# Optimization experiments

Measured on AMD Instinct MI355X. Metric: run time of the kernel, lower is better.

The kernel has to match this reference:

```python
import jax, jax.numpy as jnp
import numpy as np

D = 64          # d_model
H = 128         # ffn_hidden_dim
N = 10000       # nodes
E = 50000       # edges
NEG_SLOPE = 0.01  # LeakyReLU default


def setup_inputs() -> dict:
    key = jax.random.key(0)
    ks = jax.random.split(key, 10)
    x = jax.random.normal(ks[0], (N, D), dtype=jnp.float32)
    edge_index = jax.random.randint(ks[1], (2, E), 0, N)
    edge_attr = jax.random.normal(ks[2], (E, D), dtype=jnp.float32)
    # MapE2NxN params (stored as [in, out] so forward is x @ W + b)
    w1 = jax.random.normal(ks[3], (D, H), dtype=jnp.float32) / np.sqrt(D)
    b1 = jnp.zeros((H,), dtype=jnp.float32)
    w2 = jax.random.normal(ks[4], (H, D * D), dtype=jnp.float32) / np.sqrt(H)
    b2 = jnp.zeros((D * D,), dtype=jnp.float32)
    # NNConv root weight + bias
    root = jax.random.normal(ks[5], (D, D), dtype=jnp.float32) / np.sqrt(D)
    bias = jnp.zeros((D,), dtype=jnp.float32)
    # LayerNorm affine params
    gamma = jnp.ones((D,), dtype=jnp.float32)
    beta = jnp.zeros((D,), dtype=jnp.float32)
    return {"x": x, "edge_attr": edge_attr, "gamma": gamma, "beta": beta,
            "w1": w1, "b1": b1, "w2": w2, "b2": b2,
            "root": root, "bias": bias, "edge_index": edge_index}


def _layer_norm(h, gamma, beta, eps=1e-5):
    mu = jnp.mean(h, axis=-1, keepdims=True)
    var = jnp.var(h, axis=-1, keepdims=True)
    return (h - mu) * jax.lax.rsqrt(var + eps) * gamma + beta


def _leaky_relu(h):
    return jnp.where(h >= 0, h, NEG_SLOPE * h)


def reference(x, edge_attr, gamma, beta, w1, b1, w2, b2, root, bias, edge_index):
    src, dst = edge_index[0], edge_index[1]
    # DeepGCNLayer block='res+': pre-activation norm -> act -> (dropout p=0) -> conv -> residual
    h = _leaky_relu(_layer_norm(x, gamma, beta))
    # MapE2NxN on edge attributes -> per-edge [D, D] weight matrix
    we = _leaky_relu(edge_attr @ w1 + b1) @ w2 + b2   # [E, D*D]
    we = we.reshape(E, D, D)
    # per-edge matvec with source node features (PyG NNConv message)
    msg = jnp.einsum('ed,edf->ef', h[src], we)        # [E, D]
    # scatter-mean aggregate into destination nodes
    agg = jax.ops.segment_sum(msg, dst, num_segments=N)
    cnt = jax.ops.segment_sum(jnp.ones((E,), dtype=msg.dtype), dst, num_segments=N)
    agg = agg / jnp.maximum(cnt, 1.0)[:, None]
    # root transform + bias, then residual
    out = agg + h @ root + bias
    return x + out
```

## Files before the change

### kernel.cpp

```cpp
#include <hip/hip_runtime.h>

#define NS 10000
#define DD 64
#define HH 128
#define EE 50000
#define SLOPE 0.01f
#define BPAD 8448
#define NCH 33

typedef __attribute__((ext_vector_type(8))) short short8;
typedef __attribute__((ext_vector_type(4))) short bf4;
typedef __attribute__((ext_vector_type(4))) float f32x4;

static __device__ __forceinline__ unsigned short f2bf(float f) {
  unsigned int u = __float_as_uint(f);
  u += 0x7fff + ((u >> 16) & 1);
  return (unsigned short)(u >> 16);
}
static __device__ __forceinline__ float bf2f(unsigned short s) {
  return __uint_as_float((unsigned int)s << 16);
}
static __device__ __forceinline__ unsigned cvtpk(float lo, float hi) {
  unsigned r;
  asm("v_cvt_pk_bf16_f32 %0, %1, %2" : "=v"(r) : "v"(lo), "v"(hi));
  return r;
}

__device__ __forceinline__ float wave_sum64(float v) {
  #pragma unroll
  for (int m = 32; m >= 1; m >>= 1) v += __shfl_xor(v, m, 64);
  return v;
}

#define TBLK 128
#define PBLK 2500
#define UB 782
__global__ __launch_bounds__(256) void k_prep(const float* __restrict__ x,
    const float* __restrict__ gamma, const float* __restrict__ beta,
    float* __restrict__ h, unsigned short* __restrict__ hbf,
    const float* __restrict__ ea, const float* __restrict__ w2,
    unsigned short* __restrict__ w2e, const float* __restrict__ w1,
    const float* __restrict__ b1, unsigned short* __restrict__ ubf,
    const float* __restrict__ b2, const int* __restrict__ ei,
    int* __restrict__ cntdst) {
  __shared__ __align__(16) unsigned char smem[18432];
  int t = threadIdx.x;
  int bid = blockIdx.x;
  if (bid < TBLK) {
    float (*tile)[65] = (float(*)[65])smem;
    int k = bid;
    #pragma unroll
    for (int i = 0; i < 16; ++i) {
      int idx = t + i * 256;
      tile[idx >> 6][idx & 63] = w2[k * (DD * DD) + idx];
    }
    __syncthreads();
    #pragma unroll
    for (int it = 0; it < 2; ++it) {
      int slot = t + it * 256;
      int f = slot >> 3, l8 = slot & 7;
      short8 o;
      #pragma unroll
      for (int j = 0; j < 8; ++j) o[j] = f2bf(tile[l8 * 8 + j][f]);
      *(short8*)(w2e + (size_t)f * BPAD + k * DD + l8 * 8) = o;
    }
    return;
  }
  if (bid == TBLK) {
    #pragma unroll
    for (int i = 0; i < 16; ++i) {
      int idx = t + i * 256;
      int d = idx >> 6, f = idx & 63;
      w2e[(size_t)f * BPAD + 8192 + d] = f2bf(b2[idx]);
    }
    #pragma unroll
    for (int i = 0; i < 6; ++i) {
      int slot = t + i * 256;
      int f = slot / 24, z8 = slot % 24;
      short8 z = {};
      *(short8*)(w2e + (size_t)f * BPAD + 8256 + z8 * 8) = z;
    }
    return;
  }
  if (bid < TBLK + 1 + PBLK) {
    int pbid = bid - TBLK - 1;
    int gid = pbid * 256 + t;
    if (gid < EE) atomicAdd(&cntdst[ei[EE + gid]], 1);
    int wid = t >> 6;
    int lane = t & 63;
    int row = pbid * 4 + wid;
    if (row >= NS) return;
    float v = x[row * DD + lane];
    float s = wave_sum64(v);
    float s2 = wave_sum64(v * v);
    float mu = s * (1.0f / 64.0f);
    float var = s2 * (1.0f / 64.0f) - mu * mu;
    float r = rsqrtf(var + 1e-5f);
    float hn = (v - mu) * r * gamma[lane] + beta[lane];
    float hv = hn >= 0.f ? hn : SLOPE * hn;
    h[row * DD + lane] = hv;
    hbf[row * DD + lane] = f2bf(hv);
    return;
  }
  int ublk = bid - TBLK - 1 - PBLK;
  unsigned short (*W)[72] = (unsigned short(*)[72])smem;
  int w = t >> 6, lane = t & 63, lr = lane & 15, lg = lane >> 4;
  int r0 = ublk * 64 + w * 16;
  int ra = r0 + lr; if (ra >= EE) ra = EE - 1;
  const float* ep = ea + (size_t)ra * DD;
  float4 e0 = *(const float4*)(ep + lg * 8);
  float4 e1 = *(const float4*)(ep + lg * 8 + 4);
  float4 e2 = *(const float4*)(ep + 32 + lg * 8);
  float4 e3 = *(const float4*)(ep + 32 + lg * 8 + 4);
  #pragma unroll
  for (int i = 0; i < 32; ++i) {
    int idx = t + i * 256;
    int d = idx >> 7, hc = idx & 127;
    W[hc][d] = f2bf(w1[idx]);
  }
  __syncthreads();
  short8 a0, a1;
  a0[0] = f2bf(e0.x); a0[1] = f2bf(e0.y); a0[2] = f2bf(e0.z); a0[3] = f2bf(e0.w);
  a0[4] = f2bf(e1.x); a0[5] = f2bf(e1.y); a0[6] = f2bf(e1.z); a0[7] = f2bf(e1.w);
  a1[0] = f2bf(e2.x); a1[1] = f2bf(e2.y); a1[2] = f2bf(e2.z); a1[3] = f2bf(e2.w);
  a1[4] = f2bf(e3.x); a1[5] = f2bf(e3.y); a1[6] = f2bf(e3.z); a1[7] = f2bf(e3.w);
  short8 bb0[8], bb1[8];
  #pragma unroll
  for (int ni = 0; ni < 8; ++ni) {
    bb0[ni] = *(const short8*)(&W[ni * 16 + lr][lg * 8]);
    bb1[ni] = *(const short8*)(&W[ni * 16 + lr][32 + lg * 8]);
  }
  f32x4 acc[8] = {};
  #pragma unroll
  for (int ni = 0; ni < 8; ++ni) {
    acc[ni] = __builtin_amdgcn_mfma_f32_16x16x32_bf16(a0, bb0[ni], acc[ni], 0, 0, 0);
    acc[ni] = __builtin_amdgcn_mfma_f32_16x16x32_bf16(a1, bb1[ni], acc[ni], 0, 0, 0);
  }
  #pragma unroll
  for (int ni = 0; ni < 8; ++ni) {
    int col = ni * 16 + lr;
    float bb = b1[col];
    #pragma unroll
    for (int reg = 0; reg < 4; ++reg) {
      int gr = r0 + lg * 4 + reg;
      if (gr < EE) {
        float vv = acc[ni][reg] + bb;
        ubf[(size_t)gr * HH + col] = f2bf(vv >= 0.f ? vv : SLOPE * vv);
      }
    }
  }
}

__global__ __launch_bounds__(256) void k_msgd(
    const unsigned short* __restrict__ ubf, const float* __restrict__ hf,
    const unsigned short* __restrict__ w2e, const int* __restrict__ ei,
    float* __restrict__ agg) {
  __shared__ unsigned short Bs[64 * 256];
  int t = threadIdx.x;
  int w = t >> 6, lane = t & 63, lr = lane & 15, lg = lane >> 4;
  int cq = blockIdx.y;
  int nch = (cq == 3) ? 9 : 8;
  int ebase = (blockIdx.x * 4 + w) * 32;
  int e0 = ebase + lr, e1 = ebase + 16 + lr;
  int e0c = e0 < EE ? e0 : EE - 1;
  int e1c = e1 < EE ? e1 : EE - 1;
  int s0 = ei[e0c], s1 = ei[e1c];
  float h0[2][8], h1[2][8];
  #pragma unroll
  for (int par = 0; par < 2; ++par) {
    const float* p0 = hf + (size_t)s0 * DD + par * 32 + lg * 8;
    const float* p1 = hf + (size_t)s1 * DD + par * 32 + lg * 8;
    *(float4*)(&h0[par][0]) = *(const float4*)(p0);
    *(float4*)(&h0[par][4]) = *(const float4*)(p0 + 4);
    *(float4*)(&h1[par][0]) = *(const float4*)(p1);
    *(float4*)(&h1[par][4]) = *(const float4*)(p1 + 4);
  }
  const unsigned short* u0 = ubf + (size_t)e0c * HH;
  const unsigned short* u1 = ubf + (size_t)e1c * HH;
  int sf = (t >> 4);
  int so8 = (t & 15);
  short8 sreg[8];
  {
    int ch0 = cq * 8;
    #pragma unroll
    for (int i = 0; i < 8; ++i) {
      int f = sf + (i & 3) * 16;
      int o8 = so8 + (i >> 2) * 16;
      sreg[i] = *(const short8*)(w2e + (size_t)f * BPAD + ch0 * 256 + o8 * 8);
    }
  }
  f32x4 acc[2][4] = {};
  for (int ci = 0; ci < nch; ++ci) {
    int ch = (ci < 8) ? (cq * 8 + ci) : 32;
    __syncthreads();
    #pragma unroll
    for (int i = 0; i < 8; ++i) {
      int f = sf + (i & 3) * 16;
      int o8 = so8 + (i >> 2) * 16;
      *(short8*)(&Bs[f * 256 + (o8 ^ (f & 7)) * 8]) = sreg[i];
    }
    if (ci + 1 < nch) {
      int ch2 = (ci + 1 < 8) ? (cq * 8 + ci + 1) : 32;
      #pragma unroll
      for (int i = 0; i < 8; ++i) {
        int f = sf + (i & 3) * 16;
        int o8 = so8 + (i >> 2) * 16;
        sreg[i] = *(const short8*)(w2e + (size_t)f * BPAD + ch2 * 256 + o8 * 8);
      }
    }
    float uf0[4], uf1[4];
    if (ch < 32) {
      bf4 v0 = *(const bf4*)(u0 + ch * 4);
      bf4 v1 = *(const bf4*)(u1 + ch * 4);
      #pragma unroll
      for (int kk = 0; kk < 4; ++kk) {
        uf0[kk] = bf2f((unsigned short)v0[kk]);
        uf1[kk] = bf2f((unsigned short)v1[kk]);
      }
    } else {
      uf0[0] = 1.f; uf0[1] = 0.f; uf0[2] = 0.f; uf0[3] = 0.f;
      uf1[0] = 1.f; uf1[1] = 0.f; uf1[2] = 0.f; uf1[3] = 0.f;
    }
    __syncthreads();
    #pragma unroll
    for (int ks = 0; ks < 8; ++ks) {
      int par = ks & 1;
      float u0k = (ks >> 1) == 0 ? uf0[0] : (ks >> 1) == 1 ? uf0[1]
                 : (ks >> 1) == 2 ? uf0[2] : uf0[3];
      float u1k = (ks >> 1) == 0 ? uf1[0] : (ks >> 1) == 1 ? uf1[1]
                 : (ks >> 1) == 2 ? uf1[2] : uf1[3];
      union { unsigned u[4]; short8 s; } pk0, pk1;
      #pragma unroll
      for (int jj = 0; jj < 4; ++jj) {
        pk0.u[jj] = cvtpk(u0k * h0[par][jj * 2], u0k * h0[par][jj * 2 + 1]);
        pk1.u[jj] = cvtpk(u1k * h1[par][jj * 2], u1k * h1[par][jj * 2 + 1]);
      }
      int o8r = ks * 4 + lg;
      #pragma unroll
      for (int ft = 0; ft < 4; ++ft) {
        int f = ft * 16 + lr;
        short8 b = *(const short8*)(&Bs[f * 256 + (o8r ^ (f & 7)) * 8]);
        acc[0][ft] = __builtin_amdgcn_mfma_f32_16x16x32_bf16(pk0.s, b,
                                                             acc[0][ft], 0, 0, 0);
        acc[1][ft] = __builtin_amdgcn_mfma_f32_16x16x32_bf16(pk1.s, b,
                                                             acc[1][ft], 0, 0, 0);
      }
    }
  }
  #pragma unroll
  for (int m = 0; m < 2; ++m)
    #pragma unroll
    for (int reg = 0; reg < 4; ++reg) {
      int ee = ebase + m * 16 + lg * 4 + reg;
      if (ee < EE) {
        int dstn = ei[EE + ee];
        #pragma unroll
        for (int ft = 0; ft < 4; ++ft)
          atomicAdd(&agg[(size_t)dstn * DD + ft * 16 + lr],
                    m == 0 ? acc[0][ft][reg] : acc[1][ft][reg]);
      }
    }
}

__global__ __launch_bounds__(256) void k_final(const float* __restrict__ x,
    const float* __restrict__ h, const float* __restrict__ root,
    const float* __restrict__ bias, const float* __restrict__ agg,
    const int* __restrict__ cnt, float* __restrict__ out) {
  __shared__ float Bs[DD][DD + 1];
  __shared__ float As[32][DD];
  int t = threadIdx.x;
  #pragma unroll
  for (int i = 0; i < 16; ++i) {
    int idx = t + i * 256;
    Bs[idx >> 6][idx & 63] = root[idx];
  }
  int row0 = blockIdx.x * 32;
  #pragma unroll
  for (int i = 0; i < 8; ++i) {
    int idx = t + i * 256;
    int r = idx >> 6, d = idx & 63;
    int gr = row0 + r;
    As[r][d] = (gr < NS) ? h[gr * DD + d] : 0.f;
  }
  __syncthreads();
  int r = t >> 3;
  int c0 = (t & 7) * 8;
  int gr = row0 + r;
  if (gr >= NS) return;
  float acc[8] = {};
  for (int d = 0; d < DD; ++d) {
    float a = As[r][d];
    #pragma unroll
    for (int j = 0; j < 8; ++j) acc[j] += a * Bs[d][c0 + j];
  }
  float inv = 1.0f / fmaxf((float)cnt[gr], 1.0f);
  #pragma unroll
  for (int j = 0; j < 8; ++j) {
    size_t gi = (size_t)gr * DD + c0 + j;
    out[gi] = x[gi] + agg[gi] * inv + acc[j] + bias[c0 + j];
  }
}

extern "C" void kernel_launch(void* const* d_in, const int* in_sizes, int n_in,
                              void* d_out, int out_size, void* d_ws, size_t ws_size,
                              hipStream_t stream) {
  const float* x     = (const float*)d_in[0];
  const float* ea    = (const float*)d_in[1];
  const float* gamma = (const float*)d_in[2];
  const float* beta  = (const float*)d_in[3];
  const float* w1    = (const float*)d_in[4];
  const float* b1    = (const float*)d_in[5];
  const float* w2    = (const float*)d_in[6];
  const float* b2    = (const float*)d_in[7];
  const float* root  = (const float*)d_in[8];
  const float* bias  = (const float*)d_in[9];
  const int*   ei    = (const int*)d_in[10];
  float* out = (float*)d_out;

  char* p = (char*)d_ws;
  auto carve = [&](size_t bytes) {
    char* q = p;
    p += (bytes + 255) & ~(size_t)255;
    return q;
  };
  float* h            = (float*)carve(sizeof(float) * NS * DD);
  unsigned short* hbf = (unsigned short*)carve(sizeof(short) * NS * DD);
  unsigned short* w2e = (unsigned short*)carve(sizeof(short) * (size_t)DD * BPAD);
  unsigned short* ubf = (unsigned short*)carve(sizeof(short) * (size_t)EE * HH);
  char* z0 = p;
  float* agg          = (float*)carve(sizeof(float) * NS * DD);
  int* cntdst         = (int*)carve(sizeof(int) * NS);
  size_t zlen = (size_t)(p - z0);

  (void)hipMemsetAsync(z0, 0, zlen, stream);
  k_prep<<<dim3(TBLK + 1 + PBLK + UB), dim3(256), 0, stream>>>(
      x, gamma, beta, h, hbf, ea, w2, w2e, w1, b1, ubf, b2, ei, cntdst);
  k_msgd<<<dim3((EE + 127) / 128, 4), dim3(256), 0, stream>>>(
      ubf, h, w2e, ei, agg);
  k_final<<<dim3((NS + 31) / 32), dim3(256), 0, stream>>>(x, h, root, bias, agg,
                                                          cntdst, out);
}
```

Measured before the change: 122.3 us.

## Switch message kernel to fp16 packed products and split chunks across eight groups

Intermediates (h, u, expanded w2) are now stored as fp16 instead of bf16/fp32. The per-edge A operand is built with packed fp16 multiplies instead of fp32 multiplies plus bf16 conversion, and the MFMA becomes the f16 variant. The k_msgd grid doubles along y (8 chunk groups of 4 instead of 4 of 8), and the u values are preloaded up front, to raise parallelism and cut per-iteration conversion work. The cost is fewer MFMA chunks per block, more atomic adds into agg, and fp16 range and precision risk on u*h products.

```diff
diff --git a/kernel.cpp b/kernel.cpp
--- a/kernel.cpp
+++ b/kernel.cpp
@@ -6,10 +6,9 @@
 #define EE 50000
 #define SLOPE 0.01f
 #define BPAD 8448
-#define NCH 33
 
 typedef __attribute__((ext_vector_type(8))) short short8;
-typedef __attribute__((ext_vector_type(4))) short bf4;
+typedef __attribute__((ext_vector_type(8))) _Float16 half8;
 typedef __attribute__((ext_vector_type(4))) float f32x4;
 
 static __device__ __forceinline__ unsigned short f2bf(float f) {
@@ -17,13 +16,20 @@
   u += 0x7fff + ((u >> 16) & 1);
   return (unsigned short)(u >> 16);
 }
-static __device__ __forceinline__ float bf2f(unsigned short s) {
-  return __uint_as_float((unsigned int)s << 16);
-}
-static __device__ __forceinline__ unsigned cvtpk(float lo, float hi) {
+static __device__ __forceinline__ unsigned short f2h(float f) {
+  _Float16 v = (_Float16)f;
+  return __builtin_bit_cast(unsigned short, v);
+}
+static __device__ __forceinline__ unsigned pkmul(unsigned a, unsigned b) {
   unsigned r;
-  asm("v_cvt_pk_bf16_f32 %0, %1, %2" : "=v"(r) : "v"(lo), "v"(hi));
+  asm("v_pk_mul_f16 %0, %1, %2" : "=v"(r) : "v"(a), "v"(b));
   return r;
+}
+static __device__ __forceinline__ unsigned duplo(unsigned v) {
+  v &= 0xffffu; return v | (v << 16);
+}
+static __device__ __forceinline__ unsigned duphi(unsigned v) {
+  v >>= 16; return v | (v << 16);
 }
 
 __device__ __forceinline__ float wave_sum64(float v) {
@@ -37,10 +43,10 @@
 #define UB 782
 __global__ __launch_bounds__(256) void k_prep(const float* __restrict__ x,
     const float* __restrict__ gamma, const float* __restrict__ beta,
-    float* __restrict__ h, unsigned short* __restrict__ hbf,
+    float* __restrict__ h, unsigned short* __restrict__ h16,
     const float* __restrict__ ea, const float* __restrict__ w2,
     unsigned short* __restrict__ w2e, const float* __restrict__ w1,
-    const float* __restrict__ b1, unsigned short* __restrict__ ubf,
+    const float* __restrict__ b1, unsigned short* __restrict__ u16,
     const float* __restrict__ b2, const int* __restrict__ ei,
     int* __restrict__ cntdst) {
   __shared__ __align__(16) unsigned char smem[18432];
@@ -61,7 +67,7 @@
       int f = slot >> 3, l8 = slot & 7;
       short8 o;
       #pragma unroll
-      for (int j = 0; j < 8; ++j) o[j] = f2bf(tile[l8 * 8 + j][f]);
+      for (int j = 0; j < 8; ++j) o[j] = f2h(tile[l8 * 8 + j][f]);
       *(short8*)(w2e + (size_t)f * BPAD + k * DD + l8 * 8) = o;
     }
     return;
@@ -71,7 +77,7 @@
     for (int i = 0; i < 16; ++i) {
       int idx = t + i * 256;
       int d = idx >> 6, f = idx & 63;
-      w2e[(size_t)f * BPAD + 8192 + d] = f2bf(b2[idx]);
+      w2e[(size_t)f * BPAD + 8192 + d] = f2h(b2[idx]);
     }
     #pragma unroll
     for (int i = 0; i < 6; ++i) {
@@ -99,7 +105,7 @@
     float hn = (v - mu) * r * gamma[lane] + beta[lane];
     float hv = hn >= 0.f ? hn : SLOPE * hn;
     h[row * DD + lane] = hv;
-    hbf[row * DD + lane] = f2bf(hv);
+    h16[row * DD + lane] = f2h(hv);
     return;
   }
   int ublk = bid - TBLK - 1 - PBLK;
@@ -145,43 +151,52 @@
       int gr = r0 + lg * 4 + reg;
       if (gr < EE) {
         float vv = acc[ni][reg] + bb;
-        ubf[(size_t)gr * HH + col] = f2bf(vv >= 0.f ? vv : SLOPE * vv);
+        u16[(size_t)gr * HH + col] = f2h(vv >= 0.f ? vv : SLOPE * vv);
       }
     }
   }
 }
 
 __global__ __launch_bounds__(256) void k_msgd(
-    const unsigned short* __restrict__ ubf, const float* __restrict__ hf,
+    const unsigned short* __restrict__ u16, const unsigned short* __restrict__ h16,
     const unsigned short* __restrict__ w2e, const int* __restrict__ ei,
     float* __restrict__ agg) {
   __shared__ unsigned short Bs[64 * 256];
   int t = threadIdx.x;
   int w = t >> 6, lane = t & 63, lr = lane & 15, lg = lane >> 4;
   int cq = blockIdx.y;
-  int nch = (cq == 3) ? 9 : 8;
+  int nch = (cq == 7) ? 5 : 4;
   int ebase = (blockIdx.x * 4 + w) * 32;
   int e0 = ebase + lr, e1 = ebase + 16 + lr;
   int e0c = e0 < EE ? e0 : EE - 1;
   int e1c = e1 < EE ? e1 : EE - 1;
   int s0 = ei[e0c], s1 = ei[e1c];
-  float h0[2][8], h1[2][8];
+  unsigned hp0[2][4], hp1[2][4];
   #pragma unroll
   for (int par = 0; par < 2; ++par) {
-    const float* p0 = hf + (size_t)s0 * DD + par * 32 + lg * 8;
-    const float* p1 = hf + (size_t)s1 * DD + par * 32 + lg * 8;
-    *(float4*)(&h0[par][0]) = *(const float4*)(p0);
-    *(float4*)(&h0[par][4]) = *(const float4*)(p0 + 4);
-    *(float4*)(&h1[par][0]) = *(const float4*)(p1);
-    *(float4*)(&h1[par][4]) = *(const float4*)(p1 + 4);
-  }
-  const unsigned short* u0 = ubf + (size_t)e0c * HH;
-  const unsigned short* u1 = ubf + (size_t)e1c * HH;
-  int sf = (t >> 4);
-  int so8 = (t & 15);
+    uint4 v0 = *(const uint4*)(h16 + (size_t)s0 * DD + par * 32 + lg * 8);
+    uint4 v1 = *(const uint4*)(h16 + (size_t)s1 * DD + par * 32 + lg * 8);
+    hp0[par][0] = v0.x; hp0[par][1] = v0.y; hp0[par][2] = v0.z; hp0[par][3] = v0.w;
+    hp1[par][0] = v1.x; hp1[par][1] = v1.y; hp1[par][2] = v1.z; hp1[par][3] = v1.w;
+  }
+  uint2 uv0[5], uv1[5];
+  #pragma unroll
+  for (int ci = 0; ci < 5; ++ci) {
+    if (ci < nch) {
+      int ch = cq * 4 + ci;
+      if (ch < 32) {
+        uv0[ci] = *(const uint2*)(u16 + (size_t)e0c * HH + ch * 4);
+        uv1[ci] = *(const uint2*)(u16 + (size_t)e1c * HH + ch * 4);
+      } else {
+        uv0[ci] = make_uint2(0x3C00u, 0u);
+        uv1[ci] = make_uint2(0x3C00u, 0u);
+      }
+    }
+  }
+  int sf = t >> 4, so8 = t & 15;
   short8 sreg[8];
   {
-    int ch0 = cq * 8;
+    int ch0 = cq * 4;
     #pragma unroll
     for (int i = 0; i < 8; ++i) {
       int f = sf + (i & 3) * 16;
@@ -191,16 +206,16 @@
   }
   f32x4 acc[2][4] = {};
   for (int ci = 0; ci < nch; ++ci) {
-    int ch = (ci < 8) ? (cq * 8 + ci) : 32;
-    __syncthreads();
+    if (ci) __syncthreads();
     #pragma unroll
     for (int i = 0; i < 8; ++i) {
       int f = sf + (i & 3) * 16;
       int o8 = so8 + (i >> 2) * 16;
       *(short8*)(&Bs[f * 256 + (o8 ^ (f & 7)) * 8]) = sreg[i];
     }
+    __syncthreads();
     if (ci + 1 < nch) {
-      int ch2 = (ci + 1 < 8) ? (cq * 8 + ci + 1) : 32;
+      int ch2 = (ci + 1 < 4) ? (cq * 4 + ci + 1) : 32;
       #pragma unroll
       for (int i = 0; i < 8; ++i) {
         int f = sf + (i & 3) * 16;
@@ -208,42 +223,31 @@
         sreg[i] = *(const short8*)(w2e + (size_t)f * BPAD + ch2 * 256 + o8 * 8);
       }
     }
-    float uf0[4], uf1[4];
-    if (ch < 32) {
-      bf4 v0 = *(const bf4*)(u0 + ch * 4);
-      bf4 v1 = *(const bf4*)(u1 + ch * 4);
-      #pragma unroll
-      for (int kk = 0; kk < 4; ++kk) {
-        uf0[kk] = bf2f((unsigned short)v0[kk]);
-        uf1[kk] = bf2f((unsigned short)v1[kk]);
-      }
-    } else {
-      uf0[0] = 1.f; uf0[1] = 0.f; uf0[2] = 0.f; uf0[3] = 0.f;
-      uf1[0] = 1.f; uf1[1] = 0.f; uf1[2] = 0.f; uf1[3] = 0.f;
-    }
-    __syncthreads();
+    unsigned ud0[4], ud1[4];
+    ud0[0] = duplo(uv0[ci].x); ud0[1] = duphi(uv0[ci].x);
+    ud0[2] = duplo(uv0[ci].y); ud0[3] = duphi(uv0[ci].y);
+    ud1[0] = duplo(uv1[ci].x); ud1[1] = duphi(uv1[ci].x);
+    ud1[2] = duplo(uv1[ci].y); ud1[3] = duphi(uv1[ci].y);
     #pragma unroll
     for (int ks = 0; ks < 8; ++ks) {
-      int par = ks & 1;
-      float u0k = (ks >> 1) == 0 ? uf0[0] : (ks >> 1) == 1 ? uf0[1]
-                 : (ks >> 1) == 2 ? uf0[2] : uf0[3];
-      float u1k = (ks >> 1) == 0 ? uf1[0] : (ks >> 1) == 1 ? uf1[1]
-                 : (ks >> 1) == 2 ? uf1[2] : uf1[3];
-      union { unsigned u[4]; short8 s; } pk0, pk1;
+      int par = ks & 1, kk = ks >> 1;
+      union { unsigned u[4]; half8 h; } pa0, pa1;
       #pragma unroll
       for (int jj = 0; jj < 4; ++jj) {
-        pk0.u[jj] = cvtpk(u0k * h0[par][jj * 2], u0k * h0[par][jj * 2 + 1]);
-        pk1.u[jj] = cvtpk(u1k * h1[par][jj * 2], u1k * h1[par][jj * 2 + 1]);
+        pa0.u[jj] = pkmul(kk == 0 ? ud0[0] : kk == 1 ? ud0[1] : kk == 2 ? ud0[2] : ud0[3],
+                          hp0[par][jj]);
+        pa1.u[jj] = pkmul(kk == 0 ? ud1[0] : kk == 1 ? ud1[1] : kk == 2 ? ud1[2] : ud1[3],
+                          hp1[par][jj]);
       }
       int o8r = ks * 4 + lg;
       #pragma unroll
       for (int ft = 0; ft < 4; ++ft) {
         int f = ft * 16 + lr;
-        short8 b = *(const short8*)(&Bs[f * 256 + (o8r ^ (f & 7)) * 8]);
-        acc[0][ft] = __builtin_amdgcn_mfma_f32_16x16x32_bf16(pk0.s, b,
-                                                             acc[0][ft], 0, 0, 0);
-        acc[1][ft] = __builtin_amdgcn_mfma_f32_16x16x32_bf16(pk1.s, b,
-                                                             acc[1][ft], 0, 0, 0);
+        half8 b = *(const half8*)(&Bs[f * 256 + (o8r ^ (f & 7)) * 8]);
+        acc[0][ft] = __builtin_amdgcn_mfma_f32_16x16x32_f16(pa0.h, b,
+                                                            acc[0][ft], 0, 0, 0);
+        acc[1][ft] = __builtin_amdgcn_mfma_f32_16x16x32_f16(pa1.h, b,
+                                                            acc[1][ft], 0, 0, 0);
       }
     }
   }
@@ -324,9 +328,9 @@
     return q;
   };
   float* h            = (float*)carve(sizeof(float) * NS * DD);
-  unsigned short* hbf = (unsigned short*)carve(sizeof(short) * NS * DD);
+  unsigned short* h16 = (unsigned short*)carve(sizeof(short) * NS * DD);
   unsigned short* w2e = (unsigned short*)carve(sizeof(short) * (size_t)DD * BPAD);
-  unsigned short* ubf = (unsigned short*)carve(sizeof(short) * (size_t)EE * HH);
+  unsigned short* u16 = (unsigned short*)carve(sizeof(short) * (size_t)EE * HH);
   char* z0 = p;
   float* agg          = (float*)carve(sizeof(float) * NS * DD);
   int* cntdst         = (int*)carve(sizeof(int) * NS);
@@ -334,9 +338,9 @@
 
   (void)hipMemsetAsync(z0, 0, zlen, stream);
   k_prep<<<dim3(TBLK + 1 + PBLK + UB), dim3(256), 0, stream>>>(
-      x, gamma, beta, h, hbf, ea, w2, w2e, w1, b1, ubf, b2, ei, cntdst);
-  k_msgd<<<dim3((EE + 127) / 128, 4), dim3(256), 0, stream>>>(
-      ubf, h, w2e, ei, agg);
+      x, gamma, beta, h, h16, ea, w2, w2e, w1, b1, u16, b2, ei, cntdst);
+  k_msgd<<<dim3((EE + 127) / 128, 8), dim3(256), 0, stream>>>(
+      u16, h16, w2e, ei, agg);
   k_final<<<dim3((NS + 31) / 32), dim3(256), 0, stream>>>(x, h, root, bias, agg,
                                                           cntdst, out);
 }
```

Result: slower. 161.0 us (+31.7%).
